# Optimization experiments

Measured on AMD Instinct MI355X. Metric: run time of the kernel, lower is better.

The kernel has to match this reference:

```python
import jax, jax.numpy as jnp
import numpy as np

N_NODES = 50000
N_EDGES = 640000
D_IN = 128
D_HID = 128
D_OUT = 128
N_GRAPHS = 64


def gcn_conv(x, edge_index, W, b, n_nodes):
    """PyG GCNConv: D^{-1/2} (A + I) D^{-1/2} X W + b (unit edge weights)."""
    src, dst = edge_index[0], edge_index[1]
    h = x @ W  # [N, d_out]
    # degree counts target-side edges plus the self loop
    deg = jax.ops.segment_sum(jnp.ones_like(dst, dtype=h.dtype), dst,
                              num_segments=n_nodes) + 1.0
    dinv = jax.lax.rsqrt(deg)  # deg >= 1 so always finite
    norm = dinv[src] * dinv[dst]  # [E]
    msg = h[src] * norm[:, None]  # gather + scale  [E, d_out]
    agg = jax.ops.segment_sum(msg, dst, num_segments=n_nodes)
    # self-loop contribution: norm_ii = dinv_i^2
    agg = agg + h * (dinv * dinv)[:, None]
    return agg + b


def global_mean_pool(x, batch, n_graphs):
    sums = jax.ops.segment_sum(x, batch, num_segments=n_graphs)
    cnt = jax.ops.segment_sum(jnp.ones((x.shape[0],), dtype=x.dtype), batch,
                              num_segments=n_graphs)
    return sums / jnp.maximum(cnt, 1.0)[:, None]


def setup_inputs() -> dict:
    key = jax.random.key(0)
    k = jax.random.split(key, 8)
    x = jax.random.normal(k[0], (N_NODES, D_IN), dtype=jnp.float32)
    edge_index = jax.random.randint(k[1], (2, N_EDGES), 0, N_NODES, dtype=jnp.int64)
    batch = jnp.sort(jax.random.randint(k[2], (N_NODES,), 0, N_GRAPHS, dtype=jnp.int64))
    s1 = 1.0 / np.sqrt(D_IN)
    s2 = 1.0 / np.sqrt(D_HID)
    W1 = jax.random.uniform(k[3], (D_IN, D_HID), jnp.float32, -s1, s1)
    b1 = jnp.zeros((D_HID,), jnp.float32)
    W2 = jax.random.uniform(k[4], (D_HID, D_OUT), jnp.float32, -s2, s2)
    b2 = jnp.zeros((D_OUT,), jnp.float32)
    return {"x": x, "edge_index": edge_index, "batch": batch,
            "W1": W1, "b1": b1, "W2": W2, "b2": b2}


def reference(x, edge_index, batch, W1, b1, W2, b2):
    n = x.shape[0]
    h = jax.nn.relu(gcn_conv(x, edge_index, W1, b1, n))
    h = gcn_conv(h, edge_index, W2, b2, n)
    return global_mean_pool(h, batch, N_GRAPHS)
```

## Files before the change

kernel.cpp:

```cpp
#include <hip/hip_runtime.h>


#define D 128
#define NGRAPH 64
#define SCAN_B 1024
#define AGG_BLOCKS 2048

typedef _Float16 h16x2 __attribute__((ext_vector_type(2)));

__device__ __forceinline__ float2 h2f(unsigned u) {
    h16x2 h = __builtin_bit_cast(h16x2, u);
    return make_float2((float)h.x, (float)h.y);
}
__device__ __forceinline__ unsigned f2h(float x, float y) {
    h16x2 h;
    h.x = (_Float16)x;
    h.y = (_Float16)y;
    return __builtin_bit_cast(unsigned, h);
}

__global__ void zero_out_kernel(float* __restrict__ out, int n) {
    int i = blockIdx.x * blockDim.x + threadIdx.x;
    if (i < n) out[i] = 0.f;
}

__global__ void count_kernel(const int* __restrict__ ei, int* __restrict__ deg,
                             int E, int N) {
    int e = blockIdx.x * blockDim.x + threadIdx.x;
    if (e < E) {
        int d = ei[E + e];
        if (d >= 0 && d < N) atomicAdd(&deg[d], 1);
    }
}

__global__ __launch_bounds__(SCAN_B) void block_scan_kernel(const int* __restrict__ deg,
                                                            int* __restrict__ rowstart,
                                                            int* __restrict__ bsum,
                                                            float* __restrict__ dinv,
                                                            int N) {
    __shared__ int sc[SCAN_B];
    int t = threadIdx.x;
    int i = blockIdx.x * SCAN_B + t;
    int orig = (i < N) ? deg[i] : 0;
    int v = orig;
    sc[t] = v;
    __syncthreads();
    for (int off = 1; off < SCAN_B; off <<= 1) {
        int add = (t >= off) ? sc[t - off] : 0;
        __syncthreads();
        v += add;
        sc[t] = v;
        __syncthreads();
    }
    if (i < N) {
        rowstart[i] = v - orig;
        dinv[i]     = rsqrtf((float)orig + 1.0f);
    }
    if (t == SCAN_B - 1) bsum[blockIdx.x] = v;
}

__global__ __launch_bounds__(SCAN_B) void finalize_scan_kernel(const int* __restrict__ bsum,
                                                               int* __restrict__ rowstart,
                                                               int* __restrict__ cursor,
                                                               int N, int nblk, int E) {
    __shared__ int s_off;
    if (threadIdx.x < 64) {
        int lane = (int)threadIdx.x;
        int v = (lane < nblk && lane < (int)blockIdx.x) ? bsum[lane] : 0;
        for (int off = 32; off > 0; off >>= 1) v += __shfl_down(v, off);
        if (lane == 0) s_off = v;
    }
    __syncthreads();
    int i = blockIdx.x * SCAN_B + threadIdx.x;
    if (i < N) {
        int rs = rowstart[i] + s_off;
        rowstart[i] = rs;
        cursor[i]   = rs;
    }
    if (blockIdx.x == 0 && threadIdx.x == 0) rowstart[N] = E;
}

__global__ __launch_bounds__(256) void gemm_fill_kernel(const float* __restrict__ X,
                                                        const float* __restrict__ W,
                                                        const float* __restrict__ dinv,
                                                        unsigned* __restrict__ Gh,
                                                        const int* __restrict__ ei,
                                                        int* __restrict__ cursor,
                                                        int* __restrict__ colidx,
                                                        int N, int E, int gb) {
    __shared__ float Alds[64][D];
    if ((int)blockIdx.x >= gb) {
        int e = ((int)blockIdx.x - gb) * 256 + (int)threadIdx.x;
        if (e < E) {
            int d = ei[E + e];
            if (d >= 0 && d < N) {
                int slot = atomicAdd(&cursor[d], 1);
                if (slot >= 0 && slot < E) {
                    int s = ei[e];
                    colidx[slot] = min(max(s, 0), N - 1);
                }
            }
        }
        return;
    }

    int t = threadIdx.x;
    int row0 = blockIdx.x * 64;
    {
        int c4 = (t & 31) * 4;
        int rsub = t >> 5;
#pragma unroll
        for (int rr = 0; rr < 8; ++rr) {
            int r = rr * 8 + rsub;
            int row = row0 + r;
            if (row >= N) row = N - 1;
            float4 v = *(const float4*)(X + (size_t)row * D + c4);
            *(float4*)&Alds[r][c4] = v;
        }
    }
    __syncthreads();

    int tx = t & 31, ty = t >> 5;
    float4 acc[8];
#pragma unroll
    for (int r = 0; r < 8; ++r) acc[r] = make_float4(0.f, 0.f, 0.f, 0.f);

    for (int k = 0; k < D; ++k) {
        float4 w = *(const float4*)(W + (size_t)k * D + tx * 4);
#pragma unroll
        for (int r = 0; r < 8; ++r) {
            float a = Alds[ty * 8 + r][k];
            acc[r].x = fmaf(a, w.x, acc[r].x);
            acc[r].y = fmaf(a, w.y, acc[r].y);
            acc[r].z = fmaf(a, w.z, acc[r].z);
            acc[r].w = fmaf(a, w.w, acc[r].w);
        }
    }

#pragma unroll
    for (int r = 0; r < 8; ++r) {
        int row = row0 + ty * 8 + r;
        if (row < N) {
            float dv = dinv[row];
            uint2 o;
            o.x = f2h(dv * acc[r].x, dv * acc[r].y);
            o.y = f2h(dv * acc[r].z, dv * acc[r].w);
            *(uint2*)(Gh + (size_t)row * (D / 2) + tx * 2) = o;
        }
    }
}

__global__ __launch_bounds__(256) void agg1_kernel(const unsigned* __restrict__ Gh,
                                                   const int* __restrict__ rowstart,
                                                   const int* __restrict__ colidx,
                                                   const float* __restrict__ dinv,
                                                   const float* __restrict__ b1,
                                                   unsigned* __restrict__ Hh,
                                                   int N, int chunk) {
    int gid  = blockIdx.x * 4 + (threadIdx.x >> 6);
    int lane = threadIdx.x & 63;
    int i0 = gid * chunk, i1 = min(i0 + chunk, N);
    float bx = b1[2 * lane], by = b1[2 * lane + 1];
    for (int i = i0; i < i1; ++i) {
        float di = dinv[i];
        float2 acc = h2f(Gh[(size_t)i * (D / 2) + lane]);
        int e0 = rowstart[i], e1 = rowstart[i + 1];
        int e = e0;
        for (; e + 3 < e1; e += 4) {
            int s0 = colidx[e], s1 = colidx[e + 1];
            int s2 = colidx[e + 2], s3 = colidx[e + 3];
            unsigned u0 = Gh[(size_t)s0 * (D / 2) + lane];
            unsigned u1 = Gh[(size_t)s1 * (D / 2) + lane];
            unsigned u2 = Gh[(size_t)s2 * (D / 2) + lane];
            unsigned u3 = Gh[(size_t)s3 * (D / 2) + lane];
            float2 v0 = h2f(u0), v1 = h2f(u1), v2 = h2f(u2), v3 = h2f(u3);
            acc.x += (v0.x + v1.x) + (v2.x + v3.x);
            acc.y += (v0.y + v1.y) + (v2.y + v3.y);
        }
        for (; e < e1; ++e) {
            float2 v = h2f(Gh[(size_t)colidx[e] * (D / 2) + lane]);
            acc.x += v.x;
            acc.y += v.y;
        }
        float hx = fmaxf(fmaf(di, acc.x, bx), 0.f) * di;
        float hy = fmaxf(fmaf(di, acc.y, by), 0.f) * di;
        Hh[(size_t)i * (D / 2) + lane] = f2h(hx, hy);
    }
}

__global__ __launch_bounds__(256) void agg2_pool_kernel(const unsigned* __restrict__ Hh,
                                                        const int* __restrict__ rowstart,
                                                        const int* __restrict__ colidx,
                                                        const float* __restrict__ dinv,
                                                        const int* __restrict__ batch,
                                                        float* __restrict__ pool,
                                                        int N, int chunk) {
    int gid  = blockIdx.x * 4 + (threadIdx.x >> 6);
    int lane = threadIdx.x & 63;
    int i0 = gid * chunk, i1 = min(i0 + chunk, N);
    if (i0 >= N) return;

    float2 pa = make_float2(0.f, 0.f);
    int cur = min(max(batch[i0], 0), NGRAPH - 1);
    for (int i = i0; i < i1; ++i) {
        float di = dinv[i];
        float2 a = h2f(Hh[(size_t)i * (D / 2) + lane]);
        int e0 = rowstart[i], e1 = rowstart[i + 1];
        int e = e0;
        for (; e + 3 < e1; e += 4) {
            int s0 = colidx[e], s1 = colidx[e + 1];
            int s2 = colidx[e + 2], s3 = colidx[e + 3];
            unsigned u0 = Hh[(size_t)s0 * (D / 2) + lane];
            unsigned u1 = Hh[(size_t)s1 * (D / 2) + lane];
            unsigned u2 = Hh[(size_t)s2 * (D / 2) + lane];
            unsigned u3 = Hh[(size_t)s3 * (D / 2) + lane];
            float2 v0 = h2f(u0), v1 = h2f(u1), v2 = h2f(u2), v3 = h2f(u3);
            a.x += (v0.x + v1.x) + (v2.x + v3.x);
            a.y += (v0.y + v1.y) + (v2.y + v3.y);
        }
        for (; e < e1; ++e) {
            float2 v = h2f(Hh[(size_t)colidx[e] * (D / 2) + lane]);
            a.x += v.x;
            a.y += v.y;
        }
        int b = min(max(batch[i], 0), NGRAPH - 1);
        if (b != cur) {
            atomicAdd(&pool[(size_t)cur * D + 2 * lane], pa.x);
            atomicAdd(&pool[(size_t)cur * D + 2 * lane + 1], pa.y);
            pa = make_float2(0.f, 0.f);
            cur = b;
        }
        pa.x = fmaf(di, a.x, pa.x);
        pa.y = fmaf(di, a.y, pa.y);
    }
    atomicAdd(&pool[(size_t)cur * D + 2 * lane], pa.x);
    atomicAdd(&pool[(size_t)cur * D + 2 * lane + 1], pa.y);
}

__device__ __forceinline__ int lbound(const int* __restrict__ a, int n, int v) {
    int lo = 0, hi = n;
    while (lo < hi) {
        int m = (lo + hi) >> 1;
        if (a[m] < v) lo = m + 1; else hi = m;
    }
    return lo;
}

__global__ void final_gemm_kernel(const float* __restrict__ pool,
                                  const int* __restrict__ batch,
                                  const float* __restrict__ W2,
                                  const float* __restrict__ b2,
                                  float* __restrict__ out, int N) {
    int g = blockIdx.x, o = threadIdx.x;
    int s = lbound(batch, N, g);
    int e = lbound(batch, N, g + 1);
    float inv_cnt = 1.0f / fmaxf((float)(e - s), 1.0f);
    float acc = 0.f;
#pragma unroll 4
    for (int k = 0; k < D; ++k)
        acc = fmaf(pool[g * D + k], W2[k * D + o], acc);
    out[g * D + o] = acc * inv_cnt + b2[o];
}


extern "C" void kernel_launch(void* const* d_in, const int* in_sizes, int n_in,
                              void* d_out, int out_size, void* d_ws, size_t ws_size,
                              hipStream_t stream) {
    const float* x     = (const float*)d_in[0];
    const int*   ei    = (const int*)  d_in[1];
    const int*   batch = (const int*)  d_in[2];
    const float* W1    = (const float*)d_in[3];
    const float* b1    = (const float*)d_in[4];
    const float* W2    = (const float*)d_in[5];
    const float* b2    = (const float*)d_in[6];
    float* out = (float*)d_out;

    const int N = in_sizes[0] / D;
    const int E = in_sizes[1] / 2;
    const int nblk = (N + SCAN_B - 1) / SCAN_B;

    char* ws = (char*)d_ws;
    size_t off = 0;
    auto carve = [&](size_t bytes) {
        size_t o = off;
        off = (off + bytes + 255) & ~(size_t)255;
        return o;
    };
    size_t o_deg      = carve((size_t)N * 4);
    size_t o_pool     = carve((size_t)NGRAPH * D * 4);
    size_t zspan      = off;
    size_t o_rowstart = carve((size_t)(N + 1) * 4);
    size_t o_cursor   = carve((size_t)(N + 1) * 4);
    size_t o_dinv     = carve((size_t)N * 4);
    size_t o_colidx   = carve((size_t)E * 4);
    size_t o_bsum     = carve((size_t)64 * 4);
    size_t o_gh       = carve((size_t)N * D * 2);
    size_t o_hh       = carve((size_t)N * D * 2);
    size_t need = off;

    if (ws_size < need) {
        zero_out_kernel<<<(out_size + 255) / 256, 256, 0, stream>>>(out, out_size);
        return;
    }

    int*      deg      = (int*)     (ws + o_deg);
    float*    pool     = (float*)   (ws + o_pool);
    int*      rowstart = (int*)     (ws + o_rowstart);
    int*      cursor   = (int*)     (ws + o_cursor);
    float*    dinv     = (float*)   (ws + o_dinv);
    int*      colidx   = (int*)     (ws + o_colidx);
    int*      bsum     = (int*)     (ws + o_bsum);
    unsigned* Gh       = (unsigned*)(ws + o_gh);
    unsigned* Hh       = (unsigned*)(ws + o_hh);

    hipMemsetAsync(ws, 0, zspan, stream);

    int eb = (E + 255) / 256;
    int gb = (N + 63) / 64;
    count_kernel<<<eb, 256, 0, stream>>>(ei, deg, E, N);
    block_scan_kernel<<<nblk, SCAN_B, 0, stream>>>(deg, rowstart, bsum, dinv, N);
    finalize_scan_kernel<<<nblk, SCAN_B, 0, stream>>>(bsum, rowstart, cursor, N, nblk, E);
    gemm_fill_kernel<<<gb + eb, 256, 0, stream>>>(x, W1, dinv, Gh, ei, cursor,
                                                  colidx, N, E, gb);

    int groups = AGG_BLOCKS * 4;
    int chunk  = (N + groups - 1) / groups;
    agg1_kernel<<<AGG_BLOCKS, 256, 0, stream>>>(Gh, rowstart, colidx, dinv, b1,
                                                Hh, N, chunk);
    agg2_pool_kernel<<<AGG_BLOCKS, 256, 0, stream>>>(Hh, rowstart, colidx, dinv,
                                                     batch, pool, N, chunk);
    final_gemm_kernel<<<NGRAPH, D, 0, stream>>>(pool, batch, W2, b2, out, N);
}
```

Baseline: 242.2 us.

## Use f16 MFMA for first-layer GEMM with pre-converted inputs and 8-wide gathers

Converts X to fp16 and pre-swizzles W1 into MFMA B-fragment layout inside a fused count/convert kernel. The first GEMM then uses the 16x16x32 f16 MFMA instruction instead of scalar FP32 FMAs over LDS. The aggregation loops also gain an 8-wide unrolled gather to keep more loads in flight. The cost is an extra pass that writes a half-precision copy of X, lower input precision in the GEMM, and narrow 2-byte scattered stores of the output.

```diff
diff --git a/kernel.cpp b/kernel.cpp
--- a/kernel.cpp
+++ b/kernel.cpp
@@ -7,6 +7,8 @@
 #define AGG_BLOCKS 2048
 
 typedef _Float16 h16x2 __attribute__((ext_vector_type(2)));
+typedef _Float16 f16x8 __attribute__((ext_vector_type(8)));
+typedef float    f32x4 __attribute__((ext_vector_type(4)));
 
 __device__ __forceinline__ float2 h2f(unsigned u) {
     h16x2 h = __builtin_bit_cast(h16x2, u);
@@ -24,9 +26,39 @@
     if (i < n) out[i] = 0.f;
 }
 
-__global__ void count_kernel(const int* __restrict__ ei, int* __restrict__ deg,
-                             int E, int N) {
-    int e = blockIdx.x * blockDim.x + threadIdx.x;
+__global__ __launch_bounds__(256) void conv_count_kernel(const float* __restrict__ X,
+                                                         _Float16* __restrict__ Xh,
+                                                         const float* __restrict__ W1,
+                                                         _Float16* __restrict__ WB,
+                                                         const int* __restrict__ ei,
+                                                         int* __restrict__ deg,
+                                                         int N, int E, int cb) {
+    int b = (int)blockIdx.x;
+    if (b < cb) {
+        int idx = b * 256 + (int)threadIdx.x;
+        int total = N * (D / 4);
+        if (idx < total) {
+            float4 v = ((const float4*)X)[idx];
+            uint2 o;
+            o.x = f2h(v.x, v.y);
+            o.y = f2h(v.z, v.w);
+            ((uint2*)Xh)[idx] = o;
+        }
+        return;
+    }
+    if (b < cb + 8) {
+        int idx = (b - cb) * 256 + (int)threadIdx.x;
+        int lane = idx & 63;
+        int nt   = (idx >> 6) & 7;
+        int kt   = idx >> 9;
+        int col  = nt * 16 + (lane & 15);
+        int krow = kt * 32 + (lane >> 4) * 8;
+#pragma unroll
+        for (int j = 0; j < 8; ++j)
+            WB[idx * 8 + j] = (_Float16)W1[(krow + j) * D + col];
+        return;
+    }
+    int e = (b - cb - 8) * 256 + (int)threadIdx.x;
     if (e < E) {
         int d = ei[E + e];
         if (d >= 0 && d < N) atomicAdd(&deg[d], 1);
@@ -80,15 +112,14 @@
     if (blockIdx.x == 0 && threadIdx.x == 0) rowstart[N] = E;
 }
 
-__global__ __launch_bounds__(256) void gemm_fill_kernel(const float* __restrict__ X,
-                                                        const float* __restrict__ W,
+__global__ __launch_bounds__(256) void gemm_fill_kernel(const _Float16* __restrict__ Xh,
+                                                        const _Float16* __restrict__ WB,
                                                         const float* __restrict__ dinv,
-                                                        unsigned* __restrict__ Gh,
+                                                        _Float16* __restrict__ Gh,
                                                         const int* __restrict__ ei,
                                                         int* __restrict__ cursor,
                                                         int* __restrict__ colidx,
                                                         int N, int E, int gb) {
-    __shared__ float Alds[64][D];
     if ((int)blockIdx.x >= gb) {
         int e = ((int)blockIdx.x - gb) * 256 + (int)threadIdx.x;
         if (e < E) {
@@ -104,48 +135,40 @@
         return;
     }
 
-    int t = threadIdx.x;
-    int row0 = blockIdx.x * 64;
-    {
-        int c4 = (t & 31) * 4;
-        int rsub = t >> 5;
-#pragma unroll
-        for (int rr = 0; rr < 8; ++rr) {
-            int r = rr * 8 + rsub;
-            int row = row0 + r;
-            if (row >= N) row = N - 1;
-            float4 v = *(const float4*)(X + (size_t)row * D + c4);
-            *(float4*)&Alds[r][c4] = v;
-        }
-    }
-    __syncthreads();
-
-    int tx = t & 31, ty = t >> 5;
-    float4 acc[8];
-#pragma unroll
-    for (int r = 0; r < 8; ++r) acc[r] = make_float4(0.f, 0.f, 0.f, 0.f);
-
-    for (int k = 0; k < D; ++k) {
-        float4 w = *(const float4*)(W + (size_t)k * D + tx * 4);
-#pragma unroll
-        for (int r = 0; r < 8; ++r) {
-            float a = Alds[ty * 8 + r][k];
-            acc[r].x = fmaf(a, w.x, acc[r].x);
-            acc[r].y = fmaf(a, w.y, acc[r].y);
-            acc[r].z = fmaf(a, w.z, acc[r].z);
-            acc[r].w = fmaf(a, w.w, acc[r].w);
-        }
-    }
-
-#pragma unroll
-    for (int r = 0; r < 8; ++r) {
-        int row = row0 + ty * 8 + r;
+    int t = (int)threadIdx.x;
+    int wave = t >> 6, lane = t & 63;
+    int mbase = blockIdx.x * 64 + wave * 16;
+    int arow  = mbase + (lane & 15);
+    if (arow >= N) arow = N - 1;
+    int kgrp  = lane >> 4;
+
+    f16x8 afrag[4];
+#pragma unroll
+    for (int kt = 0; kt < 4; ++kt) {
+        uint4 u = *(const uint4*)(Xh + (size_t)arow * D + kt * 32 + kgrp * 8);
+        afrag[kt] = __builtin_bit_cast(f16x8, u);
+    }
+    f32x4 acc[8];
+#pragma unroll
+    for (int nt = 0; nt < 8; ++nt) acc[nt] = (f32x4){0.f, 0.f, 0.f, 0.f};
+#pragma unroll
+    for (int kt = 0; kt < 4; ++kt) {
+#pragma unroll
+        for (int nt = 0; nt < 8; ++nt) {
+            uint4 u = *(const uint4*)(WB + (((kt * 8 + nt) * 64 + lane) * 8));
+            f16x8 bfrag = __builtin_bit_cast(f16x8, u);
+            acc[nt] = __builtin_amdgcn_mfma_f32_16x16x32_f16(afrag[kt], bfrag, acc[nt], 0, 0, 0);
+        }
+    }
+    int r0 = mbase + kgrp * 4;
+#pragma unroll
+    for (int r = 0; r < 4; ++r) {
+        int row = r0 + r;
         if (row < N) {
             float dv = dinv[row];
-            uint2 o;
-            o.x = f2h(dv * acc[r].x, dv * acc[r].y);
-            o.y = f2h(dv * acc[r].z, dv * acc[r].w);
-            *(uint2*)(Gh + (size_t)row * (D / 2) + tx * 2) = o;
+#pragma unroll
+            for (int nt = 0; nt < 8; ++nt)
+                Gh[(size_t)row * D + nt * 16 + (lane & 15)] = (_Float16)(dv * acc[nt][r]);
         }
     }
 }
@@ -166,16 +189,29 @@
         float2 acc = h2f(Gh[(size_t)i * (D / 2) + lane]);
         int e0 = rowstart[i], e1 = rowstart[i + 1];
         int e = e0;
+        for (; e + 7 < e1; e += 8) {
+            unsigned u[8];
+#pragma unroll
+            for (int j = 0; j < 8; ++j)
+                u[j] = Gh[(size_t)colidx[e + j] * (D / 2) + lane];
+#pragma unroll
+            for (int j = 0; j < 8; ++j) {
+                float2 v = h2f(u[j]);
+                acc.x += v.x;
+                acc.y += v.y;
+            }
+        }
         for (; e + 3 < e1; e += 4) {
-            int s0 = colidx[e], s1 = colidx[e + 1];
-            int s2 = colidx[e + 2], s3 = colidx[e + 3];
-            unsigned u0 = Gh[(size_t)s0 * (D / 2) + lane];
-            unsigned u1 = Gh[(size_t)s1 * (D / 2) + lane];
-            unsigned u2 = Gh[(size_t)s2 * (D / 2) + lane];
-            unsigned u3 = Gh[(size_t)s3 * (D / 2) + lane];
-            float2 v0 = h2f(u0), v1 = h2f(u1), v2 = h2f(u2), v3 = h2f(u3);
-            acc.x += (v0.x + v1.x) + (v2.x + v3.x);
-            acc.y += (v0.y + v1.y) + (v2.y + v3.y);
+            unsigned u[4];
+#pragma unroll
+            for (int j = 0; j < 4; ++j)
+                u[j] = Gh[(size_t)colidx[e + j] * (D / 2) + lane];
+#pragma unroll
+            for (int j = 0; j < 4; ++j) {
+                float2 v = h2f(u[j]);
+                acc.x += v.x;
+                acc.y += v.y;
+            }
         }
         for (; e < e1; ++e) {
             float2 v = h2f(Gh[(size_t)colidx[e] * (D / 2) + lane]);
@@ -207,16 +243,29 @@
         float2 a = h2f(Hh[(size_t)i * (D / 2) + lane]);
         int e0 = rowstart[i], e1 = rowstart[i + 1];
         int e = e0;
+        for (; e + 7 < e1; e += 8) {
+            unsigned u[8];
+#pragma unroll
+            for (int j = 0; j < 8; ++j)
+                u[j] = Hh[(size_t)colidx[e + j] * (D / 2) + lane];
+#pragma unroll
+            for (int j = 0; j < 8; ++j) {
+                float2 v = h2f(u[j]);
+                a.x += v.x;
+                a.y += v.y;
+            }
+        }
         for (; e + 3 < e1; e += 4) {
-            int s0 = colidx[e], s1 = colidx[e + 1];
-            int s2 = colidx[e + 2], s3 = colidx[e + 3];
-            unsigned u0 = Hh[(size_t)s0 * (D / 2) + lane];
-            unsigned u1 = Hh[(size_t)s1 * (D / 2) + lane];
-            unsigned u2 = Hh[(size_t)s2 * (D / 2) + lane];
-            unsigned u3 = Hh[(size_t)s3 * (D / 2) + lane];
-            float2 v0 = h2f(u0), v1 = h2f(u1), v2 = h2f(u2), v3 = h2f(u3);
-            a.x += (v0.x + v1.x) + (v2.x + v3.x);
-            a.y += (v0.y + v1.y) + (v2.y + v3.y);
+            unsigned u[4];
+#pragma unroll
+            for (int j = 0; j < 4; ++j)
+                u[j] = Hh[(size_t)colidx[e + j] * (D / 2) + lane];
+#pragma unroll
+            for (int j = 0; j < 4; ++j) {
+                float2 v = h2f(u[j]);
+                a.x += v.x;
+                a.y += v.y;
+            }
         }
         for (; e < e1; ++e) {
             float2 v = h2f(Hh[(size_t)colidx[e] * (D / 2) + lane]);
@@ -294,6 +343,8 @@
     size_t o_dinv     = carve((size_t)N * 4);
     size_t o_colidx   = carve((size_t)E * 4);
     size_t o_bsum     = carve((size_t)64 * 4);
+    size_t o_xh       = carve((size_t)N * D * 2);
+    size_t o_wb       = carve((size_t)D * D * 2);
     size_t o_gh       = carve((size_t)N * D * 2);
     size_t o_hh       = carve((size_t)N * D * 2);
     size_t need = off;
@@ -303,31 +354,35 @@
         return;
     }
 
-    int*      deg      = (int*)     (ws + o_deg);
-    float*    pool     = (float*)   (ws + o_pool);
-    int*      rowstart = (int*)     (ws + o_rowstart);
-    int*      cursor   = (int*)     (ws + o_cursor);
-    float*    dinv     = (float*)   (ws + o_dinv);
-    int*      colidx   = (int*)     (ws + o_colidx);
-    int*      bsum     = (int*)     (ws + o_bsum);
-    unsigned* Gh       = (unsigned*)(ws + o_gh);
-    unsigned* Hh       = (unsigned*)(ws + o_hh);
+    int*       deg      = (int*)      (ws + o_deg);
+    float*     pool     = (float*)    (ws + o_pool);
+    int*       rowstart = (int*)      (ws + o_rowstart);
+    int*       cursor   = (int*)      (ws + o_cursor);
+    float*     dinv     = (float*)    (ws + o_dinv);
+    int*       colidx   = (int*)      (ws + o_colidx);
+    int*       bsum     = (int*)      (ws + o_bsum);
+    _Float16*  Xh       = (_Float16*) (ws + o_xh);
+    _Float16*  WB       = (_Float16*) (ws + o_wb);
+    _Float16*  Gh       = (_Float16*) (ws + o_gh);
+    _Float16*  Hh       = (_Float16*) (ws + o_hh);
 
     hipMemsetAsync(ws, 0, zspan, stream);
 
     int eb = (E + 255) / 256;
     int gb = (N + 63) / 64;
-    count_kernel<<<eb, 256, 0, stream>>>(ei, deg, E, N);
+    int cb = (N * (D / 4) + 255) / 256;
+
+    conv_count_kernel<<<cb + 8 + eb, 256, 0, stream>>>(x, Xh, W1, WB, ei, deg, N, E, cb);
     block_scan_kernel<<<nblk, SCAN_B, 0, stream>>>(deg, rowstart, bsum, dinv, N);
     finalize_scan_kernel<<<nblk, SCAN_B, 0, stream>>>(bsum, rowstart, cursor, N, nblk, E);
-    gemm_fill_kernel<<<gb + eb, 256, 0, stream>>>(x, W1, dinv, Gh, ei, cursor,
+    gemm_fill_kernel<<<gb + eb, 256, 0, stream>>>(Xh, WB, dinv, Gh, ei, cursor,
                                                   colidx, N, E, gb);
 
     int groups = AGG_BLOCKS * 4;
     int chunk  = (N + groups - 1) / groups;
-    agg1_kernel<<<AGG_BLOCKS, 256, 0, stream>>>(Gh, rowstart, colidx, dinv, b1,
-                                                Hh, N, chunk);
-    agg2_pool_kernel<<<AGG_BLOCKS, 256, 0, stream>>>(Hh, rowstart, colidx, dinv,
-                                                     batch, pool, N, chunk);
+    agg1_kernel<<<AGG_BLOCKS, 256, 0, stream>>>((const unsigned*)Gh, rowstart, colidx,
+                                                dinv, b1, (unsigned*)Hh, N, chunk);
+    agg2_pool_kernel<<<AGG_BLOCKS, 256, 0, stream>>>((const unsigned*)Hh, rowstart, colidx,
+                                                     dinv, batch, pool, N, chunk);
     final_gemm_kernel<<<NGRAPH, D, 0, stream>>>(pool, batch, W2, b2, out, N);
 }
```

Measured after the change: 224.2 us. 7.4% less time.
